# Kernel tuning notes

Hardware: AMD Instinct MI355X
Metric: run time of the kernel (lower is better)

## Reference

```python
import jax, jax.numpy as jnp
import numpy as np

HEADS = 12
HEAD_DIM = 64  # dim=768 // heads=12
NEG = -1e9


def setup_inputs() -> dict:
    key = jax.random.key(0)
    k1, k2, k3 = jax.random.split(key, 3)
    dim = HEADS * HEAD_DIM
    x = jax.random.normal(k1, (8, 1024, dim), dtype=jnp.float32)
    W_qkv = jax.random.normal(k2, (dim, 3 * dim), dtype=jnp.float32) * (dim ** -0.5)
    b_qkv = jnp.zeros((3 * dim,), dtype=jnp.float32)
    W_out = jax.random.normal(k3, (dim, dim), dtype=jnp.float32) * (dim ** -0.5)
    b_out = jnp.zeros((dim,), dtype=jnp.float32)
    return {"x": x, "W_qkv": W_qkv, "b_qkv": b_qkv, "W_out": W_out, "b_out": b_out}


def reference(x, W_qkv, b_qkv, W_out, b_out):
    B, T, C = x.shape
    qkv = x @ W_qkv + b_qkv                      # [B,T,3C]
    q, k, v = jnp.split(qkv, 3, axis=-1)
    # [B,T,C] -> [B,H,T,Dh]
    def split_heads(t):
        return t.reshape(B, T, HEADS, HEAD_DIM).transpose(0, 2, 1, 3)
    q, k, v = split_heads(q), split_heads(k), split_heads(v)
    att = jnp.einsum('bhqd,bhkd->bhqk', q, k) / jnp.sqrt(jnp.float32(HEAD_DIM))
    causal = jnp.tril(jnp.ones((T, T), dtype=bool))  # [T,T]
    att = jnp.where(causal[None, None], att, NEG)
    att = jax.nn.softmax(att, axis=-1)
    out = jnp.einsum('bhqk,bhkd->bhqd', att, v)  # [B,H,T,Dh]
    out = out.transpose(0, 2, 1, 3).reshape(B, T, C)
    return out @ W_out + b_out
```

## Files before the change

kernel.cpp:

```cpp
#include <hip/hip_runtime.h>
#include <hip/hip_bf16.h>

typedef unsigned short u16;
typedef unsigned int u32;
typedef __attribute__((ext_vector_type(8))) short short8;
typedef __attribute__((ext_vector_type(4))) float f32x4;
typedef __attribute__((ext_vector_type(16))) float f32x16;
typedef __attribute__((ext_vector_type(4))) unsigned int uint4v;

__device__ __forceinline__ u16 f2bf(float f) {
    union { float f; unsigned int u; } v; v.f = f;
    unsigned int u = v.u;
    return (u16)((u + 0x7FFFu + ((u >> 16) & 1u)) >> 16);
}
__device__ __forceinline__ u32 pk2(float a, float b) {
    return ((u32)f2bf(b) << 16) | (u32)f2bf(a);
}

__global__ __launch_bounds__(256) void k_prep(
    const float* __restrict__ x, u16* __restrict__ xb,
    const float* __restrict__ W_qkv, u16* __restrict__ wqt,
    const float* __restrict__ W_out, u16* __restrict__ wot)
{
    __shared__ u16 t[32][33];
    int bid = blockIdx.x, tid = threadIdx.x;
    if (bid < 6144) {
        int i = bid * 256 + tid;
        float4 v = ((const float4*)x)[i];
        ushort4 r;
        r.x = f2bf(v.x); r.y = f2bf(v.y); r.z = f2bf(v.z); r.w = f2bf(v.w);
        ((ushort4*)xb)[i] = r;
        return;
    }
    const float* W; u16* Wt; int K, N, n0, k0;
    if (bid < 7872) {
        int q = bid - 6144;
        W = W_qkv; Wt = wqt; K = 768; N = 2304;
        n0 = (q % 72) * 32; k0 = (q / 72) * 32;
    } else {
        int q = bid - 7872;
        W = W_out; Wt = wot; K = 768; N = 768;
        n0 = (q % 24) * 32; k0 = (q / 24) * 32;
    }
    int tx = tid & 31, ty = tid >> 5;
    #pragma unroll
    for (int i = 0; i < 4; i++) {
        t[ty + i * 8][tx] = f2bf(W[(long)(k0 + ty + i * 8) * N + n0 + tx]);
    }
    __syncthreads();
    #pragma unroll
    for (int i = 0; i < 4; i++) {
        Wt[(long)(n0 + ty + i * 8) * K + k0 + tx] = t[tx][ty + i * 8];
    }
}

__global__ __launch_bounds__(256) void k_vt(const u16* __restrict__ qkv, u16* __restrict__ vt) {
    __shared__ u32 s32[64][33];
    int t0 = blockIdx.x * 64, bh = blockIdx.y;
    int b = bh / 12, h = bh - b * 12;
    int tid = threadIdx.x;
    const u16* src = qkv + (size_t)(b * 1024 + t0) * 2304 + 1536 + h * 64;
    int tx = tid & 31, ty = tid >> 5;
    #pragma unroll
    for (int i = 0; i < 8; i++) {
        int t = ty + i * 8;
        s32[t][tx] = *(const u32*)&src[(size_t)t * 2304 + tx * 2];
    }
    __syncthreads();
    const u16* s16 = (const u16*)s32;
    u16* dst = vt + (size_t)bh * 65536 + t0;
    int tw = tid & 63, dw = tid >> 6;
    #pragma unroll
    for (int j = 0; j < 16; j++) {
        int d = dw + j * 4;
        dst[(size_t)d * 1024 + tw] = s16[tw * 66 + d];
    }
}

template<int EPI>
__global__ __launch_bounds__(256) void k_gemm_bt(
    const u16* __restrict__ A, const u16* __restrict__ Bt, const float* __restrict__ bias,
    float* __restrict__ Cf, u16* __restrict__ Cb,
    int M, int N, int K)
{
    __shared__ u16 lA[128][40];
    __shared__ u16 lB[128][40];
    int tid = threadIdx.x;
    int wid = tid >> 6, lane = tid & 63;
    int wm = wid >> 1, wn = wid & 1;
    int ln = lane & 15, gp = lane >> 4;
    int gm0 = blockIdx.x * 128, gn0 = blockIdx.y * 128;

    f32x4 zf = {0.f, 0.f, 0.f, 0.f};
    f32x4 acc[4][4];
    #pragma unroll
    for (int i = 0; i < 4; i++)
        #pragma unroll
        for (int j = 0; j < 4; j++) acc[i][j] = zf;

    int sr = tid >> 2;
    int sc = (tid & 3) * 8;

    for (int k0 = 0; k0 < K; k0 += 32) {
        #pragma unroll
        for (int j = 0; j < 2; j++) {
            int r = sr + j * 64;
            *(uint4v*)&lA[r][sc] = *(const uint4v*)&A[(long)(gm0 + r) * K + k0 + sc];
            *(uint4v*)&lB[r][sc] = *(const uint4v*)&Bt[(long)(gn0 + r) * K + k0 + sc];
        }
        __syncthreads();
        short8 af[4], bfr[4];
        #pragma unroll
        for (int i = 0; i < 4; i++) {
            af[i]  = *(const short8*)&lA[wm * 64 + i * 16 + ln][gp * 8];
            bfr[i] = *(const short8*)&lB[wn * 64 + i * 16 + ln][gp * 8];
        }
        #pragma unroll
        for (int i = 0; i < 4; i++)
            #pragma unroll
            for (int j = 0; j < 4; j++)
                acc[i][j] = __builtin_amdgcn_mfma_f32_16x16x32_bf16(af[i], bfr[j], acc[i][j], 0, 0, 0);
        __syncthreads();
    }

    #pragma unroll
    for (int i = 0; i < 4; i++) {
        #pragma unroll
        for (int j = 0; j < 4; j++) {
            #pragma unroll
            for (int r = 0; r < 4; r++) {
                int m = gm0 + wm * 64 + i * 16 + gp * 4 + r;
                int n = gn0 + wn * 64 + j * 16 + ln;
                float v = acc[i][j][r] + bias[n];
                if (EPI == 0) Cf[(long)m * N + n] = v;
                else          Cb[(long)m * N + n] = f2bf(v);
            }
        }
    }
}

__global__ __launch_bounds__(64, 3) void k_attn(
    const u16* __restrict__ qkv, const u16* __restrict__ Vt,
    u16* __restrict__ O)
{
    __shared__ u16 sK[2048];
    __shared__ u16 sV[2048];
    int lane = threadIdx.x;
    int l31 = lane & 31, hi = lane >> 5;
    int bx = blockIdx.x;
    int qtq = bx / 96, bh = bx - qtq * 96;
    int qt = 31 - qtq, q0 = qt * 32;
    int b = bh / 12, h = bh - b * 12;
    const u16* Qb  = qkv + (size_t)(b * 1024) * 2304 + h * 64;
    const u16* Kbb = Qb + 768;
    const u16* Vb  = Vt + (size_t)bh * 65536;

    short8 qf[4];
    #pragma unroll
    for (int ch = 0; ch < 4; ch++)
        qf[ch] = *(const short8*)&Qb[(size_t)(q0 + l31) * 2304 + ch * 16 + hi * 8];

    int rK = lane >> 3, cK = lane & 7;
    int rV = lane >> 2, cV = lane & 3;

    uint4v rk[4], rv[4];
    auto gload = [&](int kt) {
        #pragma unroll
        for (int j = 0; j < 4; j++) {
            int r = j * 8 + rK;
            rk[j] = *(const uint4v*)&Kbb[(size_t)(kt + r) * 2304 + cK * 8];
        }
        #pragma unroll
        for (int j = 0; j < 4; j++) {
            int r = j * 16 + rV;
            rv[j] = *(const uint4v*)&Vb[(size_t)r * 1024 + kt + cV * 8];
        }
    };
    auto swrite = [&]() {
        #pragma unroll
        for (int j = 0; j < 4; j++) {
            int r = j * 8 + rK;
            *(uint4v*)&sK[r * 64 + ((cK ^ (r & 7)) * 8)] = rk[j];
        }
        #pragma unroll
        for (int j = 0; j < 4; j++) {
            int r = j * 16 + rV;
            *(uint4v*)&sV[r * 32 + ((cV ^ (r & 3) ^ ((r >> 2) & 3)) * 8)] = rv[j];
        }
    };

    f32x16 o0 = {}, o1 = {};
    float mrun = -INFINITY, lsum = 0.f;
    const float SC = 0.18033688011f;
    int swl = l31 & 7;
    int swv = (l31 & 3) ^ ((l31 >> 2) & 3);

    int nit = qt + 1;
    gload(0);
    swrite();
    for (int it = 0; it < nit; it++) {
        int kt = it * 32;
        if (it + 1 < nit) gload(kt + 32);
        f32x16 sa = {}, sb = {};
        {
            short8 kf0 = *(const short8*)&sK[l31 * 64 + (((0 + hi) ^ swl) * 8)];
            short8 kf1 = *(const short8*)&sK[l31 * 64 + (((2 + hi) ^ swl) * 8)];
            short8 kf2 = *(const short8*)&sK[l31 * 64 + (((4 + hi) ^ swl) * 8)];
            short8 kf3 = *(const short8*)&sK[l31 * 64 + (((6 + hi) ^ swl) * 8)];
            sa = __builtin_amdgcn_mfma_f32_32x32x16_bf16(kf0, qf[0], sa, 0, 0, 0);
            sb = __builtin_amdgcn_mfma_f32_32x32x16_bf16(kf2, qf[2], sb, 0, 0, 0);
            sa = __builtin_amdgcn_mfma_f32_32x32x16_bf16(kf1, qf[1], sa, 0, 0, 0);
            sb = __builtin_amdgcn_mfma_f32_32x32x16_bf16(kf3, qf[3], sb, 0, 0, 0);
        }
        float raw[16];
        #pragma unroll
        for (int r = 0; r < 16; r++) raw[r] = sa[r] + sb[r];
        if (it == nit - 1) {
            #pragma unroll
            for (int r = 0; r < 16; r++) {
                int crow = (r & 3) + 8 * (r >> 2) + 4 * hi;
                raw[r] = (crow <= l31) ? raw[r] : -1e30f;
            }
        }
        float t8[8];
        #pragma unroll
        for (int i = 0; i < 8; i++) t8[i] = fmaxf(raw[i], raw[i + 8]);
        float t4a = fmaxf(t8[0], t8[1]), t4b = fmaxf(t8[2], t8[3]);
        float t4c = fmaxf(t8[4], t8[5]), t4d = fmaxf(t8[6], t8[7]);
        float tm = fmaxf(fmaxf(t4a, t4b), fmaxf(t4c, t4d));
        tm = fmaxf(tm, __shfl_xor(tm, 32));
        float stm = tm * SC;
        if (!__all(stm - mrun <= 8.0f)) {
            float mn = fmaxf(mrun, stm);
            float scale = exp2f(mrun - mn);
            lsum *= scale;
            #pragma unroll
            for (int r = 0; r < 16; r++) { o0[r] *= scale; o1[r] *= scale; }
            mrun = mn;
        }
        float ps[16];
        float rs = 0.f;
        #pragma unroll
        for (int r = 0; r < 16; r++) {
            ps[r] = exp2f(fmaf(raw[r], SC, -mrun));
            rs += ps[r];
        }
        rs += __shfl_xor(rs, 32);
        lsum += rs;
        u32 c[8], sw[8];
        #pragma unroll
        for (int i = 0; i < 8; i++) c[i] = pk2(ps[2 * i], ps[2 * i + 1]);
        #pragma unroll
        for (int i = 0; i < 8; i++) sw[i] = (u32)__shfl_xor((int)c[i], 32);
        union { u32 u[4]; short8 s8; } pb0, pb1;
        pb0.u[0] = hi ? sw[2] : c[0];
        pb0.u[1] = hi ? sw[3] : c[1];
        pb0.u[2] = hi ? c[2]  : sw[0];
        pb0.u[3] = hi ? c[3]  : sw[1];
        pb1.u[0] = hi ? sw[6] : c[4];
        pb1.u[1] = hi ? sw[7] : c[5];
        pb1.u[2] = hi ? c[6]  : sw[4];
        pb1.u[3] = hi ? c[7]  : sw[5];
        #pragma unroll
        for (int kh = 0; kh < 2; kh++) {
            const short8* pbp = kh ? &pb1.s8 : &pb0.s8;
            int p = (((kh * 2 + hi) ^ swv) * 8);
            short8 vf0 = *(const short8*)&sV[l31 * 32 + p];
            short8 vf1 = *(const short8*)&sV[(32 + l31) * 32 + p];
            o0 = __builtin_amdgcn_mfma_f32_32x32x16_bf16(vf0, *pbp, o0, 0, 0, 0);
            o1 = __builtin_amdgcn_mfma_f32_32x32x16_bf16(vf1, *pbp, o1, 0, 0, 0);
        }
        if (it + 1 < nit) swrite();
    }

    float inv = 1.0f / lsum;
    int t = q0 + l31;
    size_t base = ((size_t)(b * 1024 + t)) * 768 + h * 64;
    #pragma unroll
    for (int rq = 0; rq < 4; rq++) {
        ushort4 u0, u1;
        u0.x = f2bf(o0[4 * rq + 0] * inv); u0.y = f2bf(o0[4 * rq + 1] * inv);
        u0.z = f2bf(o0[4 * rq + 2] * inv); u0.w = f2bf(o0[4 * rq + 3] * inv);
        u1.x = f2bf(o1[4 * rq + 0] * inv); u1.y = f2bf(o1[4 * rq + 1] * inv);
        u1.z = f2bf(o1[4 * rq + 2] * inv); u1.w = f2bf(o1[4 * rq + 3] * inv);
        *(ushort4*)&O[base + rq * 8 + hi * 4]      = u0;
        *(ushort4*)&O[base + 32 + rq * 8 + hi * 4] = u1;
    }
}

extern "C" void kernel_launch(void* const* d_in, const int* in_sizes, int n_in,
                              void* d_out, int out_size, void* d_ws, size_t ws_size,
                              hipStream_t stream)
{
    const float* x     = (const float*)d_in[0];
    const float* W_qkv = (const float*)d_in[1];
    const float* b_qkv = (const float*)d_in[2];
    const float* W_out = (const float*)d_in[3];
    const float* b_out = (const float*)d_in[4];
    float* out = (float*)d_out;

    char* w = (char*)d_ws;
    u16* xb   = (u16*)w; w += (size_t)8192 * 768 * 2;
    u16* wqt  = (u16*)w; w += (size_t)2304 * 768 * 2;
    u16* wot  = (u16*)w; w += (size_t)768 * 768 * 2;
    u16* qkv  = (u16*)w; w += (size_t)8192 * 2304 * 2;
    u16* vt   = (u16*)w; w += (size_t)96 * 64 * 1024 * 2;
    u16* ao   = (u16*)w; w += (size_t)8192 * 768 * 2;

    k_prep<<<dim3(8448), 256, 0, stream>>>(x, xb, W_qkv, wqt, W_out, wot);
    k_gemm_bt<2><<<dim3(64, 18), 256, 0, stream>>>(xb, wqt, b_qkv, nullptr, qkv, 8192, 2304, 768);
    k_vt<<<dim3(16, 96), 256, 0, stream>>>(qkv, vt);
    k_attn<<<dim3(3072), 64, 0, stream>>>(qkv, vt, ao);
    k_gemm_bt<0><<<dim3(64, 6), 256, 0, stream>>>(ao, wot, b_out, out, nullptr, 8192, 768, 768);
}
```

Measured before the change: 131.9 us.

## Share K/V tiles across two query-tile waves per attention block

```diff
diff --git a/kernel.cpp b/kernel.cpp
--- a/kernel.cpp
+++ b/kernel.cpp
@@ -139,17 +139,22 @@
     }
 }
 
-__global__ __launch_bounds__(64, 3) void k_attn(
+__global__ __launch_bounds__(128) void k_attn(
     const u16* __restrict__ qkv, const u16* __restrict__ Vt,
     u16* __restrict__ O)
 {
     __shared__ u16 sK[2048];
     __shared__ u16 sV[2048];
-    int lane = threadIdx.x;
+    int tid = threadIdx.x;
+    int wv = tid >> 6;
+    int lane = tid & 63;
     int l31 = lane & 31, hi = lane >> 5;
     int bx = blockIdx.x;
-    int qtq = bx / 96, bh = bx - qtq * 96;
-    int qt = 31 - qtq, q0 = qt * 32;
+    int p = bx / 96, bh = bx - p * 96;
+    int qt = (wv == 0) ? (31 - 2 * p) : (30 - 2 * p);
+    int q0 = qt * 32;
+    int my_nit = qt + 1;
+    int nit_max = 32 - 2 * p;
     int b = bh / 12, h = bh - b * 12;
     const u16* Qb  = qkv + (size_t)(b * 1024) * 2304 + h * 64;
     const u16* Kbb = Qb + 768;
@@ -163,29 +168,35 @@
     int rK = lane >> 3, cK = lane & 7;
     int rV = lane >> 2, cV = lane & 3;
 
-    uint4v rk[4], rv[4];
+    uint4v rg[4];
     auto gload = [&](int kt) {
-        #pragma unroll
-        for (int j = 0; j < 4; j++) {
-            int r = j * 8 + rK;
-            rk[j] = *(const uint4v*)&Kbb[(size_t)(kt + r) * 2304 + cK * 8];
-        }
-        #pragma unroll
-        for (int j = 0; j < 4; j++) {
-            int r = j * 16 + rV;
-            rv[j] = *(const uint4v*)&Vb[(size_t)r * 1024 + kt + cV * 8];
+        if (wv == 0) {
+            #pragma unroll
+            for (int j = 0; j < 4; j++) {
+                int r = j * 8 + rK;
+                rg[j] = *(const uint4v*)&Kbb[(size_t)(kt + r) * 2304 + cK * 8];
+            }
+        } else {
+            #pragma unroll
+            for (int j = 0; j < 4; j++) {
+                int r = j * 16 + rV;
+                rg[j] = *(const uint4v*)&Vb[(size_t)r * 1024 + kt + cV * 8];
+            }
         }
     };
     auto swrite = [&]() {
-        #pragma unroll
-        for (int j = 0; j < 4; j++) {
-            int r = j * 8 + rK;
-            *(uint4v*)&sK[r * 64 + ((cK ^ (r & 7)) * 8)] = rk[j];
-        }
-        #pragma unroll
-        for (int j = 0; j < 4; j++) {
-            int r = j * 16 + rV;
-            *(uint4v*)&sV[r * 32 + ((cV ^ (r & 3) ^ ((r >> 2) & 3)) * 8)] = rv[j];
+        if (wv == 0) {
+            #pragma unroll
+            for (int j = 0; j < 4; j++) {
+                int r = j * 8 + rK;
+                *(uint4v*)&sK[r * 64 + ((cK ^ (r & 7)) * 8)] = rg[j];
+            }
+        } else {
+            #pragma unroll
+            for (int j = 0; j < 4; j++) {
+                int r = j * 16 + rV;
+                *(uint4v*)&sV[r * 32 + ((cV ^ (r & 3) ^ ((r >> 2) & 3)) * 8)] = rg[j];
+            }
         }
     };
 
@@ -195,82 +206,88 @@
     int swl = l31 & 7;
     int swv = (l31 & 3) ^ ((l31 >> 2) & 3);
 
-    int nit = qt + 1;
     gload(0);
     swrite();
-    for (int it = 0; it < nit; it++) {
+    __syncthreads();
+    for (int it = 0; it < nit_max; it++) {
         int kt = it * 32;
-        if (it + 1 < nit) gload(kt + 32);
-        f32x16 sa = {}, sb = {};
-        {
-            short8 kf0 = *(const short8*)&sK[l31 * 64 + (((0 + hi) ^ swl) * 8)];
-            short8 kf1 = *(const short8*)&sK[l31 * 64 + (((2 + hi) ^ swl) * 8)];
-            short8 kf2 = *(const short8*)&sK[l31 * 64 + (((4 + hi) ^ swl) * 8)];
-            short8 kf3 = *(const short8*)&sK[l31 * 64 + (((6 + hi) ^ swl) * 8)];
-            sa = __builtin_amdgcn_mfma_f32_32x32x16_bf16(kf0, qf[0], sa, 0, 0, 0);
-            sb = __builtin_amdgcn_mfma_f32_32x32x16_bf16(kf2, qf[2], sb, 0, 0, 0);
-            sa = __builtin_amdgcn_mfma_f32_32x32x16_bf16(kf1, qf[1], sa, 0, 0, 0);
-            sb = __builtin_amdgcn_mfma_f32_32x32x16_bf16(kf3, qf[3], sb, 0, 0, 0);
-        }
-        float raw[16];
-        #pragma unroll
-        for (int r = 0; r < 16; r++) raw[r] = sa[r] + sb[r];
-        if (it == nit - 1) {
+        if (it + 1 < nit_max) gload(kt + 32);
+        if (it < my_nit) {
+            f32x16 sa = {}, sb = {};
+            {
+                short8 kf0 = *(const short8*)&sK[l31 * 64 + (((0 + hi) ^ swl) * 8)];
+                short8 kf1 = *(const short8*)&sK[l31 * 64 + (((2 + hi) ^ swl) * 8)];
+                short8 kf2 = *(const short8*)&sK[l31 * 64 + (((4 + hi) ^ swl) * 8)];
+                short8 kf3 = *(const short8*)&sK[l31 * 64 + (((6 + hi) ^ swl) * 8)];
+                sa = __builtin_amdgcn_mfma_f32_32x32x16_bf16(kf0, qf[0], sa, 0, 0, 0);
+                sb = __builtin_amdgcn_mfma_f32_32x32x16_bf16(kf2, qf[2], sb, 0, 0, 0);
+                sa = __builtin_amdgcn_mfma_f32_32x32x16_bf16(kf1, qf[1], sa, 0, 0, 0);
+                sb = __builtin_amdgcn_mfma_f32_32x32x16_bf16(kf3, qf[3], sb, 0, 0, 0);
+            }
+            float raw[16];
+            #pragma unroll
+            for (int r = 0; r < 16; r++) raw[r] = sa[r] + sb[r];
+            if (it == my_nit - 1) {
+                #pragma unroll
+                for (int r = 0; r < 16; r++) {
+                    int crow = (r & 3) + 8 * (r >> 2) + 4 * hi;
+                    raw[r] = (crow <= l31) ? raw[r] : -1e30f;
+                }
+            }
+            float t8[8];
+            #pragma unroll
+            for (int i = 0; i < 8; i++) t8[i] = fmaxf(raw[i], raw[i + 8]);
+            float t4a = fmaxf(t8[0], t8[1]), t4b = fmaxf(t8[2], t8[3]);
+            float t4c = fmaxf(t8[4], t8[5]), t4d = fmaxf(t8[6], t8[7]);
+            float tm = fmaxf(fmaxf(t4a, t4b), fmaxf(t4c, t4d));
+            tm = fmaxf(tm, __shfl_xor(tm, 32));
+            float stm = tm * SC;
+            if (!__all(stm - mrun <= 8.0f)) {
+                float mn = fmaxf(mrun, stm);
+                float scale = exp2f(mrun - mn);
+                lsum *= scale;
+                #pragma unroll
+                for (int r = 0; r < 16; r++) { o0[r] *= scale; o1[r] *= scale; }
+                mrun = mn;
+            }
+            float ps[16];
+            float rs = 0.f;
             #pragma unroll
             for (int r = 0; r < 16; r++) {
-                int crow = (r & 3) + 8 * (r >> 2) + 4 * hi;
-                raw[r] = (crow <= l31) ? raw[r] : -1e30f;
-            }
-        }
-        float t8[8];
-        #pragma unroll
-        for (int i = 0; i < 8; i++) t8[i] = fmaxf(raw[i], raw[i + 8]);
-        float t4a = fmaxf(t8[0], t8[1]), t4b = fmaxf(t8[2], t8[3]);
-        float t4c = fmaxf(t8[4], t8[5]), t4d = fmaxf(t8[6], t8[7]);
-        float tm = fmaxf(fmaxf(t4a, t4b), fmaxf(t4c, t4d));
-        tm = fmaxf(tm, __shfl_xor(tm, 32));
-        float stm = tm * SC;
-        if (!__all(stm - mrun <= 8.0f)) {
-            float mn = fmaxf(mrun, stm);
-            float scale = exp2f(mrun - mn);
-            lsum *= scale;
-            #pragma unroll
-            for (int r = 0; r < 16; r++) { o0[r] *= scale; o1[r] *= scale; }
-            mrun = mn;
-        }
-        float ps[16];
-        float rs = 0.f;
-        #pragma unroll
-        for (int r = 0; r < 16; r++) {
-            ps[r] = exp2f(fmaf(raw[r], SC, -mrun));
-            rs += ps[r];
-        }
-        rs += __shfl_xor(rs, 32);
-        lsum += rs;
-        u32 c[8], sw[8];
-        #pragma unroll
-        for (int i = 0; i < 8; i++) c[i] = pk2(ps[2 * i], ps[2 * i + 1]);
-        #pragma unroll
-        for (int i = 0; i < 8; i++) sw[i] = (u32)__shfl_xor((int)c[i], 32);
-        union { u32 u[4]; short8 s8; } pb0, pb1;
-        pb0.u[0] = hi ? sw[2] : c[0];
-        pb0.u[1] = hi ? sw[3] : c[1];
-        pb0.u[2] = hi ? c[2]  : sw[0];
-        pb0.u[3] = hi ? c[3]  : sw[1];
-        pb1.u[0] = hi ? sw[6] : c[4];
-        pb1.u[1] = hi ? sw[7] : c[5];
-        pb1.u[2] = hi ? c[6]  : sw[4];
-        pb1.u[3] = hi ? c[7]  : sw[5];
-        #pragma unroll
-        for (int kh = 0; kh < 2; kh++) {
-            const short8* pbp = kh ? &pb1.s8 : &pb0.s8;
-            int p = (((kh * 2 + hi) ^ swv) * 8);
-            short8 vf0 = *(const short8*)&sV[l31 * 32 + p];
-            short8 vf1 = *(const short8*)&sV[(32 + l31) * 32 + p];
-            o0 = __builtin_amdgcn_mfma_f32_32x32x16_bf16(vf0, *pbp, o0, 0, 0, 0);
-            o1 = __builtin_amdgcn_mfma_f32_32x32x16_bf16(vf1, *pbp, o1, 0, 0, 0);
-        }
-        if (it + 1 < nit) swrite();
+                ps[r] = exp2f(fmaf(raw[r], SC, -mrun));
+                rs += ps[r];
+            }
+            rs += __shfl_xor(rs, 32);
+            lsum += rs;
+            u32 c[8], sw[8];
+            #pragma unroll
+            for (int i = 0; i < 8; i++) c[i] = pk2(ps[2 * i], ps[2 * i + 1]);
+            #pragma unroll
+            for (int i = 0; i < 8; i++) sw[i] = (u32)__shfl_xor((int)c[i], 32);
+            union { u32 u[4]; short8 s8; } pb0, pb1;
+            pb0.u[0] = hi ? sw[2] : c[0];
+            pb0.u[1] = hi ? sw[3] : c[1];
+            pb0.u[2] = hi ? c[2]  : sw[0];
+            pb0.u[3] = hi ? c[3]  : sw[1];
+            pb1.u[0] = hi ? sw[6] : c[4];
+            pb1.u[1] = hi ? sw[7] : c[5];
+            pb1.u[2] = hi ? c[6]  : sw[4];
+            pb1.u[3] = hi ? c[7]  : sw[5];
+            #pragma unroll
+            for (int kh = 0; kh < 2; kh++) {
+                const short8* pbp = kh ? &pb1.s8 : &pb0.s8;
+                int pp = (((kh * 2 + hi) ^ swv) * 8);
+                short8 vf0 = *(const short8*)&sV[l31 * 32 + pp];
+                short8 vf1 = *(const short8*)&sV[(32 + l31) * 32 + pp];
+                o0 = __builtin_amdgcn_mfma_f32_32x32x16_bf16(vf0, *pbp, o0, 0, 0, 0);
+                o1 = __builtin_amdgcn_mfma_f32_32x32x16_bf16(vf1, *pbp, o1, 0, 0, 0);
+            }
+        }
+        __syncthreads();
+        if (it + 1 < nit_max) {
+            swrite();
+            __syncthreads();
+        }
     }
 
     float inv = 1.0f / lsum;
@@ -310,6 +327,6 @@
     k_prep<<<dim3(8448), 256, 0, stream>>>(x, xb, W_qkv, wqt, W_out, wot);
     k_gemm_bt<2><<<dim3(64, 18), 256, 0, stream>>>(xb, wqt, b_qkv, nullptr, qkv, 8192, 2304, 768);
     k_vt<<<dim3(16, 96), 256, 0, stream>>>(qkv, vt);
-    k_attn<<<dim3(3072), 64, 0, stream>>>(qkv, vt, ao);
+    k_attn<<<dim3(1536), 128, 0, stream>>>(qkv, vt, ao);
     k_gemm_bt<0><<<dim3(64, 6), 256, 0, stream>>>(ao, wot, b_out, out, nullptr, 8192, 768, 768);
 }
```

Measured after the change: 133.5 us. No clear change (+1.2%).
